# Kernel optimization log

Hardware: AMD Instinct MI355X
Metric: run time of the kernel (lower is better)

Reference implementation:

```python
import jax, jax.numpy as jnp
import numpy as np
from jax.scipy.linalg import solve_triangular

EPS = 2e-05  # module eps (only used on Cholesky failure in torch; cov is PD here since M >> N)


def setup_inputs() -> dict:
    key = jax.random.key(0)
    k1, k2, k3 = jax.random.split(key, 3)
    B, N, H, W = 8, 512, 64, 64
    return {
        "cont_feat": jax.random.normal(k1, (B, N, H, W), dtype=jnp.float32),
        "styl_feat": jax.random.normal(k2, (B, N, H, W), dtype=jnp.float32),
        "x_real": jax.random.normal(k3, (B, N, H, W), dtype=jnp.float32),
    }


def reference(cont_feat, styl_feat, x_real):
    B, N, cH, cW = cont_feat.shape
    xc = cont_feat.reshape(B, N, -1)   # [B, N, Mc]
    xs = styl_feat.reshape(B, N, -1)   # [B, N, Ms]
    # x_real is reshaped in the original but never used by whitening()

    # whitening: center, covariance, Cholesky, inv(L) @ x (as triangular solve)
    xc_c = xc - jnp.mean(xc, axis=-1, keepdims=True)
    cov_c = jnp.einsum('bnm,bkm->bnk', xc_c, xc_c) / (xc_c.shape[-1] - 1)  # [B,N,N]
    Lc = jnp.linalg.cholesky(cov_c)
    whiten = solve_triangular(Lc, xc_c, lower=True)  # == inv(Lc) @ xc_c

    # coloring: style covariance Cholesky, Ls @ whiten + style mean
    xs_mean = jnp.mean(xs, axis=-1, keepdims=True)
    xs_c = xs - xs_mean
    cov_s = jnp.einsum('bnm,bkm->bnk', xs_c, xs_c) / (xs_c.shape[-1] - 1)
    Ls = jnp.linalg.cholesky(cov_s)
    out = jnp.einsum('bnk,bkm->bnm', Ls, whiten) + xs_mean
    return out.reshape(B, N, cH, cW)
```

## Files before the change

kernel.cpp:

```cpp
#include <hip/hip_runtime.h>
#include <stdint.h>


using short8   = __attribute__((ext_vector_type(8))) short;
using short4_t = __attribute__((ext_vector_type(4))) short;
using f32x4    = __attribute__((ext_vector_type(4))) float;

#define DEVI static __device__ __forceinline__

DEVI uint16_t f32_to_bf16(float f) {
  union { float f; uint32_t u; } v{f};
  uint32_t u = v.u;
  return (uint16_t)((u + 0x7fffu + ((u >> 16) & 1u)) >> 16);
}

DEVI f32x4 mfma16(short8 a, short8 b, f32x4 c) {
  return __builtin_amdgcn_mfma_f32_16x16x32_bf16(a, b, c, 0, 0, 0);
}

typedef __attribute__((address_space(3))) uint32_t lds_u32;
typedef __attribute__((address_space(1))) const uint32_t gmem_u32;

DEVI void async_cp16(const uint16_t* g, uint16_t* l) {
  __builtin_amdgcn_global_load_lds((gmem_u32*)g, (lds_u32*)l, 16, 0, 0);
}

DEVI void stage_tile(const uint16_t* __restrict__ src, int stride,
                     uint16_t* lds, int tid) {
  int w64 = (tid >> 6) << 6;
  #pragma unroll
  for (int i = 0; i < 4; ++i) {
    int f = i * 256 + tid;
    int r = f >> 3, s = f & 7;
    int c = s ^ (r & 7);
    async_cp16(src + r * stride + c * 8, lds + (i * 256 + w64) * 8);
  }
}

DEVI short8 frag_ld(const uint16_t* lds, int r, int ch) {
  return *(const short8*)(lds + r * 64 + ((ch ^ (r & 7)) * 8));
}

__global__ __launch_bounds__(256) void k_meanconv(
    const float* __restrict__ cont, const float* __restrict__ styl,
    uint16_t* __restrict__ Yc, uint16_t* __restrict__ Ys, float* __restrict__ mus) {
  int rid = blockIdx.x;
  int row = rid & 4095;
  bool is_s = rid >= 4096;
  const float* src = (is_s ? styl : cont) + (size_t)row * 4096;
  uint16_t* dst = (is_s ? Ys : Yc) + (size_t)row * 4096;
  int tid = threadIdx.x, lane = tid & 63, w = tid >> 6;

  float4 v[4];
  #pragma unroll
  for (int i = 0; i < 4; ++i) v[i] = ((const float4*)src)[i * 256 + tid];
  float s = 0.f;
  #pragma unroll
  for (int i = 0; i < 4; ++i) s += v[i].x + v[i].y + v[i].z + v[i].w;
  #pragma unroll
  for (int off = 32; off > 0; off >>= 1) s += __shfl_down(s, off);
  __shared__ float red[4];
  if (lane == 0) red[w] = s;
  __syncthreads();
  float mean = (red[0] + red[1] + red[2] + red[3]) * (1.0f / 4096.0f);
  if (is_s && tid == 0) mus[row] = mean;

  #pragma unroll
  for (int i = 0; i < 4; ++i) {
    short4_t o;
    o[0] = (short)f32_to_bf16(v[i].x - mean);
    o[1] = (short)f32_to_bf16(v[i].y - mean);
    o[2] = (short)f32_to_bf16(v[i].z - mean);
    o[3] = (short)f32_to_bf16(v[i].w - mean);
    ((short4_t*)dst)[i * 256 + tid] = o;
  }
}

__global__ __launch_bounds__(256) void k_cov(const uint16_t* __restrict__ Y,
                                             float* __restrict__ covA) {
  int bx = blockIdx.x;
  int mat = bx / 10, q = bx % 10;
  int it = (q >= 6) ? 3 : (q >= 3) ? 2 : (q >= 1) ? 1 : 0;
  int jt = q - it * (it + 1) / 2;
  const uint16_t* A = Y + (size_t)mat * 2097152;
  float* C = covA + (size_t)mat * 262144;
  __shared__ uint16_t Al[128 * 64], Bl[128 * 64];
  int tid = threadIdx.x, lane = tid & 63, w = tid >> 6;
  int wr = w >> 1, wc = w & 1, m16 = lane & 15, q4 = lane >> 4;

  f32x4 acc[4][4] = {};
  for (int kb = 0; kb < 64; ++kb) {
    __syncthreads();
    stage_tile(A + it * 128 * 4096 + kb * 64, 4096, Al, tid);
    stage_tile(A + jt * 128 * 4096 + kb * 64, 4096, Bl, tid);
    __syncthreads();
    #pragma unroll
    for (int ks = 0; ks < 2; ++ks) {
      short8 af[4], bg[4];
      #pragma unroll
      for (int t = 0; t < 4; ++t) af[t] = frag_ld(Al, wr * 64 + t * 16 + m16, ks * 4 + q4);
      #pragma unroll
      for (int t = 0; t < 4; ++t) bg[t] = frag_ld(Bl, wc * 64 + t * 16 + m16, ks * 4 + q4);
      #pragma unroll
      for (int i2 = 0; i2 < 4; ++i2)
        #pragma unroll
        for (int j2 = 0; j2 < 4; ++j2)
          acc[i2][j2] = mfma16(af[i2], bg[j2], acc[i2][j2]);
    }
  }
  const float sc = 1.0f / 4095.0f;
  #pragma unroll
  for (int t = 0; t < 4; ++t)
    #pragma unroll
    for (int u = 0; u < 4; ++u)
      #pragma unroll
      for (int g = 0; g < 4; ++g) {
        int row = it * 128 + wr * 64 + t * 16 + q4 * 4 + g;
        int col = jt * 128 + wc * 64 + u * 16 + m16;
        C[row * 512 + col] = acc[t][u][g] * sc;
      }
}

__global__ __launch_bounds__(512) void k_chol(float* __restrict__ covA,
                                              uint16_t* __restrict__ L16) {
  int mat = blockIdx.x;
  float* C = covA + (size_t)mat * 262144;
  uint16_t* L = L16 + (size_t)mat * 262144;
  __shared__ float P[512 * 36];
  __shared__ uint16_t Pb[512 * 40];
  __shared__ uint16_t Mb[32 * 40];
  int tid = threadIdx.x, lane = tid & 63, w = tid >> 6;
  int m16 = lane & 15, q4 = lane >> 4;

  for (int j = 0; j < 16; ++j) {
    int c0 = j * 32, n = 512 - c0;

    for (int e = tid; e < n * 8; e += 512) {
      int r = e >> 3, c4 = e & 7;
      *(float4*)&P[r * 36 + c4 * 4] =
          *(const float4*)(C + (size_t)(c0 + r) * 512 + c0 + c4 * 4);
    }
    __syncthreads();

    if (w == 0) {
      if (c0 > 0) {
        f32x4 t00 = {}, t10 = {}, t11 = {};
        const uint16_t* L0 = L + (size_t)(c0 + m16) * 512;
        const uint16_t* L1r = L + (size_t)(c0 + 16 + m16) * 512;
        for (int kk = 0; kk < c0; kk += 32) {
          short8 f0 = *(const short8*)(L0 + kk + q4 * 8);
          short8 f1 = *(const short8*)(L1r + kk + q4 * 8);
          t00 = mfma16(f0, f0, t00);
          t10 = mfma16(f1, f0, t10);
          t11 = mfma16(f1, f1, t11);
        }
        #pragma unroll
        for (int g = 0; g < 4; ++g) {
          int r0 = q4 * 4 + g;
          P[r0 * 36 + m16]              -= t00[g];
          P[(16 + r0) * 36 + m16]       -= t10[g];
          P[(16 + r0) * 36 + 16 + m16]  -= t11[g];
        }
      }
      if (lane < 32) {
        int r = lane;
        float a[32];
        #pragma unroll
        for (int c4 = 0; c4 < 8; ++c4) {
          float4 v = *(const float4*)&P[r * 36 + c4 * 4];
          a[c4 * 4 + 0] = v.x; a[c4 * 4 + 1] = v.y;
          a[c4 * 4 + 2] = v.z; a[c4 * 4 + 3] = v.w;
        }
        float myinv = 0.f;
        #pragma unroll
        for (int t = 0; t < 32; ++t) {
          float pv  = __shfl(a[t], t);
          float inv = __builtin_amdgcn_rsqf(pv);
          a[t] *= inv;
          if (r == t) myinv = inv;
          float scv = a[t];
          #pragma unroll
          for (int c = t + 1; c < 32; ++c)
            a[c] -= scv * __shfl(scv, c);
        }
        float xv[32];
        #pragma unroll
        for (int c = 0; c < 32; ++c) xv[c] = (c <= r) ? a[c] : 0.0f;
        float* Cw = C + (size_t)(c0 + r) * 512 + c0;
        uint16_t* Lw = L + (size_t)(c0 + r) * 512 + c0;
        #pragma unroll
        for (int c4 = 0; c4 < 8; ++c4)
          *(float4*)(Cw + c4 * 4) = make_float4(xv[c4 * 4], xv[c4 * 4 + 1],
                                                xv[c4 * 4 + 2], xv[c4 * 4 + 3]);
        #pragma unroll
        for (int c8 = 0; c8 < 4; ++c8) {
          short8 o;
          #pragma unroll
          for (int u = 0; u < 8; ++u) o[u] = (short)f32_to_bf16(xv[c8 * 8 + u]);
          *(short8*)(Lw + c8 * 8) = o;
        }
        if (n > 32) {
          float b[32];
          #pragma unroll
          for (int c = 0; c < 32; ++c) b[c] = (c == r) ? myinv : 0.0f;
          #pragma unroll
          for (int m = 0; m < 31; ++m) {
            float coef = a[m] * myinv;
            #pragma unroll
            for (int c = 0; c <= m; ++c) {
              float v = __shfl(b[c], m);
              if (r > m) b[c] -= coef * v;
            }
          }
          uint16_t* Mw = Mb + r * 40;
          #pragma unroll
          for (int c8 = 0; c8 < 4; ++c8) {
            short8 o;
            #pragma unroll
            for (int u = 0; u < 8; ++u) o[u] = (short)f32_to_bf16(b[c8 * 8 + u]);
            *(short8*)(Mw + c8 * 8) = o;
          }
        }
      }
    } else {
      int ntiles = (n - 32) >> 4;
      const uint16_t* B0 = L + (size_t)(c0 + m16) * 512;
      const uint16_t* B1 = L + (size_t)(c0 + 16 + m16) * 512;
      for (int t = w - 1; t < ntiles; t += 7) {
        f32x4 acc0 = {}, acc1 = {};
        const uint16_t* Ar = L + (size_t)(c0 + 32 + t * 16 + m16) * 512;
        for (int kk = 0; kk < c0; kk += 32) {
          short8 af = *(const short8*)(Ar + kk + q4 * 8);
          short8 b0 = *(const short8*)(B0 + kk + q4 * 8);
          short8 b1 = *(const short8*)(B1 + kk + q4 * 8);
          acc0 = mfma16(af, b0, acc0);
          acc1 = mfma16(af, b1, acc1);
        }
        #pragma unroll
        for (int g = 0; g < 4; ++g) {
          int pr = 32 + t * 16 + q4 * 4 + g;
          float v0 = P[pr * 36 + m16]      - acc0[g];
          float v1 = P[pr * 36 + 16 + m16] - acc1[g];
          Pb[pr * 40 + m16]      = f32_to_bf16(v0);
          Pb[pr * 40 + 16 + m16] = f32_to_bf16(v1);
        }
      }
    }
    __syncthreads();

    if (n > 32) {
      int ntiles = (n - 32) >> 4;
      short8 bm0 = *(const short8*)(Mb + m16 * 40 + q4 * 8);
      short8 bm1 = *(const short8*)(Mb + (16 + m16) * 40 + q4 * 8);
      for (int t = w; t < ntiles; t += 8) {
        short8 af = *(const short8*)(Pb + (size_t)(32 + t * 16 + m16) * 40 + q4 * 8);
        f32x4 x0 = {}, x1 = {};
        x0 = mfma16(af, bm0, x0);
        x1 = mfma16(af, bm1, x1);
        #pragma unroll
        for (int g = 0; g < 4; ++g) {
          int gr = c0 + 32 + t * 16 + q4 * 4 + g;
          float v0 = x0[g], v1 = x1[g];
          C[(size_t)gr * 512 + c0 + m16]      = v0;
          C[(size_t)gr * 512 + c0 + 16 + m16] = v1;
          L[(size_t)gr * 512 + c0 + m16]      = f32_to_bf16(v0);
          L[(size_t)gr * 512 + c0 + 16 + m16] = f32_to_bf16(v1);
        }
      }
    }
  }
}

__global__ __launch_bounds__(256) void k_trinv(const float* __restrict__ covA,
                                               uint16_t* __restrict__ Ut) {
  int bx = blockIdx.x;
  int matb = bx >> 5;
  int sub = bx & 31;
  int cb = sub >> 2, colgrp = sub & 3;
  const float* Lm = covA + (size_t)matb * 262144;
  uint16_t* U = Ut + (size_t)matb * 262144;
  int tid = threadIdx.x, lane = tid & 63, w = tid >> 6;
  int j = cb * 64 + colgrp * 16 + w * 4;

  __shared__ float Bl[64 * 66];
  __shared__ float Xl[4][4][512];

  for (int rb = cb; rb < 8; ++rb) {
    float acc[4];
    #pragma unroll
    for (int c = 0; c < 4; ++c) acc[c] = ((rb * 64 + lane) == (j + c)) ? 1.0f : 0.0f;
    for (int pb = cb; pb < rb; ++pb) {
      __syncthreads();
      for (int e = tid; e < 4096; e += 256)
        Bl[(e >> 6) * 66 + (e & 63)] = Lm[(rb * 64 + (e >> 6)) * 512 + pb * 64 + (e & 63)];
      __syncthreads();
      #pragma unroll 4
      for (int m = 0; m < 64; m += 2) {
        float2 b2 = *(const float2*)&Bl[lane * 66 + m];
        #pragma unroll
        for (int c = 0; c < 4; ++c)
          acc[c] -= b2.x * Xl[w][c][pb * 64 + m] + b2.y * Xl[w][c][pb * 64 + m + 1];
      }
    }
    __syncthreads();
    for (int e = tid; e < 4096; e += 256)
      Bl[(e >> 6) * 66 + (e & 63)] = Lm[(rb * 64 + (e >> 6)) * 512 + rb * 64 + (e & 63)];
    __syncthreads();
    float invd = __builtin_amdgcn_rcpf(Bl[lane * 66 + lane]);
    #pragma unroll 1
    for (int i = 0; i < 64; ++i) {
      float bcol = Bl[lane * 66 + i];
      if (lane == i) {
        #pragma unroll
        for (int c = 0; c < 4; ++c) acc[c] *= invd;
      }
      float xi[4];
      #pragma unroll
      for (int c = 0; c < 4; ++c) xi[c] = __shfl(acc[c], i);
      if (lane > i) {
        #pragma unroll
        for (int c = 0; c < 4; ++c) acc[c] -= bcol * xi[c];
      }
    }
    #pragma unroll
    for (int c = 0; c < 4; ++c) {
      Xl[w][c][rb * 64 + lane] = acc[c];
      U[(j + c) * 512 + rb * 64 + lane] = f32_to_bf16(acc[c]);
    }
  }
}

__global__ __launch_bounds__(256) void k_tprod(const uint16_t* __restrict__ Ls16,
                                               const uint16_t* __restrict__ Ut16,
                                               uint16_t* __restrict__ T16) {
  int bx = blockIdx.x;
  int b = bx / 10, q = bx % 10;
  int it = (q >= 6) ? 3 : (q >= 3) ? 2 : (q >= 1) ? 1 : 0;
  int jt = q - it * (it + 1) / 2;
  const uint16_t* A = Ls16 + (size_t)b * 262144;
  const uint16_t* B = Ut16 + (size_t)b * 262144;
  uint16_t* C = T16 + (size_t)b * 262144;
  __shared__ uint16_t Al[128 * 64], Bl[128 * 64];
  int tid = threadIdx.x, lane = tid & 63, w = tid >> 6;
  int wr = w >> 1, wc = w & 1, m16 = lane & 15, q4 = lane >> 4;

  f32x4 acc[4][4] = {};
  for (int kb = jt * 2; kb < (it + 1) * 2; ++kb) {
    __syncthreads();
    stage_tile(A + it * 128 * 512 + kb * 64, 512, Al, tid);
    stage_tile(B + jt * 128 * 512 + kb * 64, 512, Bl, tid);
    __syncthreads();
    #pragma unroll
    for (int ks = 0; ks < 2; ++ks) {
      short8 af[4], bg[4];
      #pragma unroll
      for (int t = 0; t < 4; ++t) af[t] = frag_ld(Al, wr * 64 + t * 16 + m16, ks * 4 + q4);
      #pragma unroll
      for (int t = 0; t < 4; ++t) bg[t] = frag_ld(Bl, wc * 64 + t * 16 + m16, ks * 4 + q4);
      #pragma unroll
      for (int i2 = 0; i2 < 4; ++i2)
        #pragma unroll
        for (int j2 = 0; j2 < 4; ++j2)
          acc[i2][j2] = mfma16(af[i2], bg[j2], acc[i2][j2]);
    }
  }
  #pragma unroll
  for (int t = 0; t < 4; ++t)
    #pragma unroll
    for (int u = 0; u < 4; ++u)
      #pragma unroll
      for (int g = 0; g < 4; ++g) {
        int row = it * 128 + wr * 64 + t * 16 + q4 * 4 + g;
        int col = jt * 128 + wc * 64 + u * 16 + m16;
        C[row * 512 + col] = f32_to_bf16(acc[t][u][g]);
      }
}

__global__ __launch_bounds__(256) void k_out(const uint16_t* __restrict__ T16,
                                             const uint16_t* __restrict__ Ycb,
                                             const float* __restrict__ mus,
                                             float* __restrict__ out) {
  int bx = blockIdx.x;
  int b = bx >> 7, q = bx & 127;
  int it = q >> 5, mt = q & 31;
  int m0 = mt * 128;
  const uint16_t* Tm = T16 + (size_t)b * 262144;
  const uint16_t* Y = Ycb + (size_t)b * 2097152;
  __shared__ uint16_t Al[128 * 64];
  __shared__ uint16_t Bt[128 * 68];
  int tid = threadIdx.x, lane = tid & 63, w = tid >> 6;
  int wr = w >> 1, wc = w & 1, m16 = lane & 15, q4 = lane >> 4;

  f32x4 acc[4][4] = {};
  int kbmax = (it + 1) * 2;
  for (int kb = 0; kb < kbmax; ++kb) {
    __syncthreads();
    stage_tile(Tm + it * 128 * 512 + kb * 64, 512, Al, tid);
    #pragma unroll
    for (int rep = 0; rep < 2; ++rep) {
      int task = rep * 256 + tid;
      int n8 = task & 15, kp = task >> 4;
      const uint16_t* p = Y + (size_t)(kb * 64 + 2 * kp) * 4096 + m0 + n8 * 8;
      short8 a0 = *(const short8*)p;
      short8 a1 = *(const short8*)(p + 4096);
      #pragma unroll
      for (int u = 0; u < 8; ++u) {
        int n = n8 * 8 + u;
        uint32_t pk = (uint32_t)(uint16_t)a0[u] | ((uint32_t)(uint16_t)a1[u] << 16);
        *(uint32_t*)(Bt + n * 68 + 2 * kp) = pk;
      }
    }
    __syncthreads();
    #pragma unroll
    for (int ks = 0; ks < 2; ++ks) {
      short8 af[4], bg[4];
      #pragma unroll
      for (int t = 0; t < 4; ++t) af[t] = frag_ld(Al, wr * 64 + t * 16 + m16, ks * 4 + q4);
      #pragma unroll
      for (int t = 0; t < 4; ++t) {
        int n = wc * 64 + t * 16 + m16;
        int ko = ks * 4 + q4;
        short8 bb;
        ((short4_t*)&bb)[0] = *(const short4_t*)(Bt + n * 68 + ko * 8);
        ((short4_t*)&bb)[1] = *(const short4_t*)(Bt + n * 68 + ko * 8 + 4);
        bg[t] = bb;
      }
      #pragma unroll
      for (int i2 = 0; i2 < 4; ++i2)
        #pragma unroll
        for (int j2 = 0; j2 < 4; ++j2)
          acc[i2][j2] = mfma16(af[i2], bg[j2], acc[i2][j2]);
    }
  }
  #pragma unroll
  for (int t = 0; t < 4; ++t)
    #pragma unroll
    for (int g = 0; g < 4; ++g) {
      int row = it * 128 + wr * 64 + t * 16 + q4 * 4 + g;
      float mu = mus[b * 512 + row];
      #pragma unroll
      for (int u = 0; u < 4; ++u) {
        int col = m0 + wc * 64 + u * 16 + m16;
        out[(size_t)(b * 512 + row) * 4096 + col] = acc[t][u][g] + mu;
      }
    }
}

extern "C" void kernel_launch(void* const* d_in, const int* in_sizes, int n_in,
                              void* d_out, int out_size, void* d_ws, size_t ws_size,
                              hipStream_t stream) {
  const float* cont = (const float*)d_in[0];
  const float* styl = (const float*)d_in[1];
  float* out = (float*)d_out;
  char* ws = (char*)d_ws;

  uint16_t* Ycb  = (uint16_t*)(ws);
  float*    covA = (float*)(ws + 67108864);
  uint16_t* L16  = (uint16_t*)(ws + 83886080);
  uint16_t* Ut16 = (uint16_t*)(ws + 92274688);
  uint16_t* T16  = (uint16_t*)(ws + 96468992);
  float*    mus  = (float*)(ws + 100663296);

  uint16_t* Ysb  = Ycb + 16777216;
  uint16_t* Ls16 = L16 + 8 * 262144;

  hipMemsetAsync((void*)L16, 0, 16777216, stream);

  k_meanconv<<<dim3(8192), dim3(256), 0, stream>>>(cont, styl, Ycb, Ysb, mus);
  k_cov     <<<dim3(160),  dim3(256), 0, stream>>>(Ycb, covA);
  k_chol    <<<dim3(16),   dim3(512), 0, stream>>>(covA, L16);
  k_trinv   <<<dim3(256),  dim3(256), 0, stream>>>(covA, Ut16);
  k_tprod   <<<dim3(80),   dim3(256), 0, stream>>>(Ls16, Ut16, T16);
  k_out     <<<dim3(1024), dim3(256), 0, stream>>>(T16, Ycb, mus, out);
}
```

Measured before the change: 726.8 us.

## Restructure Cholesky panel: drop full panel staging, batch tiles per wave, prefetch

```diff
diff --git a/kernel.cpp b/kernel.cpp
--- a/kernel.cpp
+++ b/kernel.cpp
@@ -126,48 +126,68 @@
   int mat = blockIdx.x;
   float* C = covA + (size_t)mat * 262144;
   uint16_t* L = L16 + (size_t)mat * 262144;
-  __shared__ float P[512 * 36];
+  __shared__ float Pd[32 * 36];
   __shared__ uint16_t Pb[512 * 40];
   __shared__ uint16_t Mb[32 * 40];
   int tid = threadIdx.x, lane = tid & 63, w = tid >> 6;
   int m16 = lane & 15, q4 = lane >> 4;
 
   for (int j = 0; j < 16; ++j) {
-    int c0 = j * 32, n = 512 - c0;
-
-    for (int e = tid; e < n * 8; e += 512) {
-      int r = e >> 3, c4 = e & 7;
-      *(float4*)&P[r * 36 + c4 * 4] =
-          *(const float4*)(C + (size_t)(c0 + r) * 512 + c0 + c4 * 4);
-    }
-    __syncthreads();
+    int c0 = j * 32;
+    int nb = (480 - 32 * j) >> 4;
+
+    int trow[5]; int myn = 0;
+    #pragma unroll
+    for (int i = 0; i < 5; ++i) {
+      int t = (w - 1) + i * 7;
+      trow[i] = c0 + 32 + t * 16;
+      if (w >= 1 && t < nb) myn = i + 1;
+    }
 
     if (w == 0) {
+      float4 pdv[4];
+      #pragma unroll
+      for (int i2 = 0; i2 < 4; ++i2) {
+        int e = i2 * 64 + lane, r = e >> 3, c4 = e & 7;
+        pdv[i2] = *(const float4*)(C + (size_t)(c0 + r) * 512 + c0 + c4 * 4);
+      }
+      f32x4 t00 = {}, t10 = {}, t11 = {};
       if (c0 > 0) {
-        f32x4 t00 = {}, t10 = {}, t11 = {};
-        const uint16_t* L0 = L + (size_t)(c0 + m16) * 512;
-        const uint16_t* L1r = L + (size_t)(c0 + 16 + m16) * 512;
+        const uint16_t* L0  = L + (size_t)(c0 + m16) * 512 + q4 * 8;
+        const uint16_t* L1r = L + (size_t)(c0 + 16 + m16) * 512 + q4 * 8;
+        short8 f0 = *(const short8*)(L0);
+        short8 f1 = *(const short8*)(L1r);
+        short8 g0, g1;
         for (int kk = 0; kk < c0; kk += 32) {
-          short8 f0 = *(const short8*)(L0 + kk + q4 * 8);
-          short8 f1 = *(const short8*)(L1r + kk + q4 * 8);
+          bool more = (kk + 32) < c0;
+          if (more) {
+            g0 = *(const short8*)(L0 + kk + 32);
+            g1 = *(const short8*)(L1r + kk + 32);
+          }
           t00 = mfma16(f0, f0, t00);
           t10 = mfma16(f1, f0, t10);
           t11 = mfma16(f1, f1, t11);
-        }
-        #pragma unroll
-        for (int g = 0; g < 4; ++g) {
-          int r0 = q4 * 4 + g;
-          P[r0 * 36 + m16]              -= t00[g];
-          P[(16 + r0) * 36 + m16]       -= t10[g];
-          P[(16 + r0) * 36 + 16 + m16]  -= t11[g];
-        }
+          if (more) { f0 = g0; f1 = g1; }
+        }
+      }
+      #pragma unroll
+      for (int i2 = 0; i2 < 4; ++i2) {
+        int e = i2 * 64 + lane, r = e >> 3, c4 = e & 7;
+        *(float4*)&Pd[r * 36 + c4 * 4] = pdv[i2];
+      }
+      #pragma unroll
+      for (int g = 0; g < 4; ++g) {
+        int r0 = q4 * 4 + g;
+        Pd[r0 * 36 + m16]             -= t00[g];
+        Pd[(16 + r0) * 36 + m16]      -= t10[g];
+        Pd[(16 + r0) * 36 + 16 + m16] -= t11[g];
       }
       if (lane < 32) {
         int r = lane;
         float a[32];
         #pragma unroll
         for (int c4 = 0; c4 < 8; ++c4) {
-          float4 v = *(const float4*)&P[r * 36 + c4 * 4];
+          float4 v = *(const float4*)&Pd[r * 36 + c4 * 4];
           a[c4 * 4 + 0] = v.x; a[c4 * 4 + 1] = v.y;
           a[c4 * 4 + 2] = v.z; a[c4 * 4 + 3] = v.w;
         }
@@ -199,7 +219,7 @@
           for (int u = 0; u < 8; ++u) o[u] = (short)f32_to_bf16(xv[c8 * 8 + u]);
           *(short8*)(Lw + c8 * 8) = o;
         }
-        if (n > 32) {
+        if (nb > 0) {
           float b[32];
           #pragma unroll
           for (int c = 0; c < 32; ++c) b[c] = (c == r) ? myinv : 0.0f;
@@ -222,44 +242,73 @@
           }
         }
       }
-    } else {
-      int ntiles = (n - 32) >> 4;
-      const uint16_t* B0 = L + (size_t)(c0 + m16) * 512;
-      const uint16_t* B1 = L + (size_t)(c0 + 16 + m16) * 512;
-      for (int t = w - 1; t < ntiles; t += 7) {
-        f32x4 acc0 = {}, acc1 = {};
-        const uint16_t* Ar = L + (size_t)(c0 + 32 + t * 16 + m16) * 512;
+    } else if (myn > 0) {
+      float po0[5][4], po1[5][4];
+      #pragma unroll
+      for (int i = 0; i < 5; ++i) if (i < myn) {
+        #pragma unroll
+        for (int g = 0; g < 4; ++g) {
+          const float* cr = C + (size_t)(trow[i] + q4 * 4 + g) * 512 + c0;
+          po0[i][g] = cr[m16];
+          po1[i][g] = cr[16 + m16];
+        }
+      }
+      f32x4 acc0[5] = {}, acc1[5] = {};
+      if (c0 > 0) {
+        const uint16_t* Lb0 = L + (size_t)(c0 + m16) * 512 + q4 * 8;
+        const uint16_t* Lb1 = L + (size_t)(c0 + 16 + m16) * 512 + q4 * 8;
+        short8 cb0 = *(const short8*)(Lb0);
+        short8 cb1 = *(const short8*)(Lb1);
+        short8 ca[5], na[5];
+        short8 nb0c, nb1c;
+        #pragma unroll
+        for (int i = 0; i < 5; ++i) if (i < myn)
+          ca[i] = *(const short8*)(L + (size_t)(trow[i] + m16) * 512 + q4 * 8);
         for (int kk = 0; kk < c0; kk += 32) {
-          short8 af = *(const short8*)(Ar + kk + q4 * 8);
-          short8 b0 = *(const short8*)(B0 + kk + q4 * 8);
-          short8 b1 = *(const short8*)(B1 + kk + q4 * 8);
-          acc0 = mfma16(af, b0, acc0);
-          acc1 = mfma16(af, b1, acc1);
-        }
+          bool more = (kk + 32) < c0;
+          if (more) {
+            nb0c = *(const short8*)(Lb0 + kk + 32);
+            nb1c = *(const short8*)(Lb1 + kk + 32);
+            #pragma unroll
+            for (int i = 0; i < 5; ++i) if (i < myn)
+              na[i] = *(const short8*)(L + (size_t)(trow[i] + m16) * 512 + kk + 32 + q4 * 8);
+          }
+          #pragma unroll
+          for (int i = 0; i < 5; ++i) if (i < myn) {
+            acc0[i] = mfma16(ca[i], cb0, acc0[i]);
+            acc1[i] = mfma16(ca[i], cb1, acc1[i]);
+          }
+          if (more) {
+            cb0 = nb0c; cb1 = nb1c;
+            #pragma unroll
+            for (int i = 0; i < 5; ++i) ca[i] = na[i];
+          }
+        }
+      }
+      #pragma unroll
+      for (int i = 0; i < 5; ++i) if (i < myn) {
         #pragma unroll
         for (int g = 0; g < 4; ++g) {
-          int pr = 32 + t * 16 + q4 * 4 + g;
-          float v0 = P[pr * 36 + m16]      - acc0[g];
-          float v1 = P[pr * 36 + 16 + m16] - acc1[g];
-          Pb[pr * 40 + m16]      = f32_to_bf16(v0);
-          Pb[pr * 40 + 16 + m16] = f32_to_bf16(v1);
-        }
-      }
-    }
-    __syncthreads();
-
-    if (n > 32) {
-      int ntiles = (n - 32) >> 4;
+          int pr = trow[i] - c0 + q4 * 4 + g;
+          Pb[pr * 40 + m16]      = f32_to_bf16(po0[i][g] - acc0[i][g]);
+          Pb[pr * 40 + 16 + m16] = f32_to_bf16(po1[i][g] - acc1[i][g]);
+        }
+      }
+    }
+    __syncthreads();
+
+    if (myn > 0) {
       short8 bm0 = *(const short8*)(Mb + m16 * 40 + q4 * 8);
       short8 bm1 = *(const short8*)(Mb + (16 + m16) * 40 + q4 * 8);
-      for (int t = w; t < ntiles; t += 8) {
-        short8 af = *(const short8*)(Pb + (size_t)(32 + t * 16 + m16) * 40 + q4 * 8);
+      #pragma unroll
+      for (int i = 0; i < 5; ++i) if (i < myn) {
+        short8 af = *(const short8*)(Pb + (size_t)(trow[i] - c0 + m16) * 40 + q4 * 8);
         f32x4 x0 = {}, x1 = {};
         x0 = mfma16(af, bm0, x0);
         x1 = mfma16(af, bm1, x1);
         #pragma unroll
         for (int g = 0; g < 4; ++g) {
-          int gr = c0 + 32 + t * 16 + q4 * 4 + g;
+          int gr = trow[i] + q4 * 4 + g;
           float v0 = x0[g], v1 = x1[g];
           C[(size_t)gr * 512 + c0 + m16]      = v0;
           C[(size_t)gr * 512 + c0 + 16 + m16] = v1;
@@ -268,6 +317,7 @@
         }
       }
     }
+    __syncthreads();
   }
 }
 
```

After: 794.7 us. 1.09x slower.

## Split-K covariance GEMM, fuse block inverse into Cholesky panel, prefetch L loads

Applied to the files above, without the earlier changes.

```diff
diff --git a/kernel.cpp b/kernel.cpp
--- a/kernel.cpp
+++ b/kernel.cpp
@@ -76,10 +76,12 @@
   }
 }
 
-__global__ __launch_bounds__(256) void k_cov(const uint16_t* __restrict__ Y,
-                                             float* __restrict__ covA) {
+__global__ __launch_bounds__(256) void k_covp(const uint16_t* __restrict__ Y,
+                                              float* __restrict__ covA,
+                                              float* __restrict__ covB) {
   int bx = blockIdx.x;
-  int mat = bx / 10, q = bx % 10;
+  int split = bx & 1, rest = bx >> 1;
+  int mat = rest / 10, q = rest % 10;
   int it = (q >= 6) ? 3 : (q >= 3) ? 2 : (q >= 1) ? 1 : 0;
   int jt = q - it * (it + 1) / 2;
   const uint16_t* A = Y + (size_t)mat * 2097152;
@@ -89,7 +91,7 @@
   int wr = w >> 1, wc = w & 1, m16 = lane & 15, q4 = lane >> 4;
 
   f32x4 acc[4][4] = {};
-  for (int kb = 0; kb < 64; ++kb) {
+  for (int kb = split * 32; kb < split * 32 + 32; ++kb) {
     __syncthreads();
     stage_tile(A + it * 128 * 4096 + kb * 64, 4096, Al, tid);
     stage_tile(A + jt * 128 * 4096 + kb * 64, 4096, Bl, tid);
@@ -109,16 +111,44 @@
     }
   }
   const float sc = 1.0f / 4095.0f;
-  #pragma unroll
-  for (int t = 0; t < 4; ++t)
-    #pragma unroll
-    for (int u = 0; u < 4; ++u)
-      #pragma unroll
-      for (int g = 0; g < 4; ++g) {
-        int row = it * 128 + wr * 64 + t * 16 + q4 * 4 + g;
-        int col = jt * 128 + wc * 64 + u * 16 + m16;
-        C[row * 512 + col] = acc[t][u][g] * sc;
-      }
+  if (split == 0) {
+    #pragma unroll
+    for (int t = 0; t < 4; ++t)
+      #pragma unroll
+      for (int u = 0; u < 4; ++u)
+        #pragma unroll
+        for (int g = 0; g < 4; ++g) {
+          int row = it * 128 + wr * 64 + t * 16 + q4 * 4 + g;
+          int col = jt * 128 + wc * 64 + u * 16 + m16;
+          C[row * 512 + col] = acc[t][u][g] * sc;
+        }
+  } else {
+    float* Bp = covB + (size_t)rest * 16384;
+    #pragma unroll
+    for (int t = 0; t < 4; ++t)
+      #pragma unroll
+      for (int u = 0; u < 4; ++u)
+        #pragma unroll
+        for (int g = 0; g < 4; ++g) {
+          int row = wr * 64 + t * 16 + q4 * 4 + g;
+          int col = wc * 64 + u * 16 + m16;
+          Bp[row * 128 + col] = acc[t][u][g] * sc;
+        }
+  }
+}
+
+__global__ __launch_bounds__(256) void k_covfix(float* __restrict__ covA,
+                                                const float* __restrict__ covB) {
+  int bx = blockIdx.x;
+  int mat = bx / 10, q = bx % 10;
+  int it = (q >= 6) ? 3 : (q >= 3) ? 2 : (q >= 1) ? 1 : 0;
+  int jt = q - it * (it + 1) / 2;
+  float* C = covA + (size_t)mat * 262144;
+  const float* Bp = covB + (size_t)bx * 16384;
+  for (int e = threadIdx.x; e < 16384; e += 256) {
+    int r = e >> 7, c = e & 127;
+    C[(it * 128 + r) * 512 + jt * 128 + c] += Bp[e];
+  }
 }
 
 __global__ __launch_bounds__(512) void k_chol(float* __restrict__ covA,
@@ -145,14 +175,18 @@
     if (w == 0) {
       if (c0 > 0) {
         f32x4 t00 = {}, t10 = {}, t11 = {};
-        const uint16_t* L0 = L + (size_t)(c0 + m16) * 512;
-        const uint16_t* L1r = L + (size_t)(c0 + 16 + m16) * 512;
+        const uint16_t* L0  = L + (size_t)(c0 + m16) * 512 + q4 * 8;
+        const uint16_t* L1r = L + (size_t)(c0 + 16 + m16) * 512 + q4 * 8;
+        short8 f0 = *(const short8*)(L0);
+        short8 f1 = *(const short8*)(L1r);
         for (int kk = 0; kk < c0; kk += 32) {
-          short8 f0 = *(const short8*)(L0 + kk + q4 * 8);
-          short8 f1 = *(const short8*)(L1r + kk + q4 * 8);
+          int kn = (kk + 32 < c0) ? kk + 32 : kk;
+          short8 g0 = *(const short8*)(L0 + kn);
+          short8 g1 = *(const short8*)(L1r + kn);
           t00 = mfma16(f0, f0, t00);
           t10 = mfma16(f1, f0, t10);
           t11 = mfma16(f1, f1, t11);
+          f0 = g0; f1 = g1;
         }
         #pragma unroll
         for (int g = 0; g < 4; ++g) {
@@ -164,6 +198,7 @@
       }
       if (lane < 32) {
         int r = lane;
+        bool needM = (n > 32);
         float a[32];
         #pragma unroll
         for (int c4 = 0; c4 < 8; ++c4) {
@@ -171,17 +206,27 @@
           a[c4 * 4 + 0] = v.x; a[c4 * 4 + 1] = v.y;
           a[c4 * 4 + 2] = v.z; a[c4 * 4 + 3] = v.w;
         }
-        float myinv = 0.f;
+        float s_[32], Mrow[32];
+        #pragma unroll
+        for (int c = 0; c < 32; ++c) { s_[c] = 0.f; Mrow[c] = 0.f; }
         #pragma unroll
         for (int t = 0; t < 32; ++t) {
           float pv  = __shfl(a[t], t);
           float inv = __builtin_amdgcn_rsqf(pv);
           a[t] *= inv;
-          if (r == t) myinv = inv;
           float scv = a[t];
           #pragma unroll
           for (int c = t + 1; c < 32; ++c)
             a[c] -= scv * __shfl(scv, c);
+          if (needM) {
+            #pragma unroll
+            for (int c = 0; c <= t; ++c) {
+              float fin = (((c == t) ? 1.0f : 0.0f) - s_[c]) * inv;
+              float mvt = __shfl(fin, t);
+              if (r == t) Mrow[c] = fin;
+              if (r > t) s_[c] += a[t] * mvt;
+            }
+          }
         }
         float xv[32];
         #pragma unroll
@@ -199,42 +244,37 @@
           for (int u = 0; u < 8; ++u) o[u] = (short)f32_to_bf16(xv[c8 * 8 + u]);
           *(short8*)(Lw + c8 * 8) = o;
         }
-        if (n > 32) {
-          float b[32];
-          #pragma unroll
-          for (int c = 0; c < 32; ++c) b[c] = (c == r) ? myinv : 0.0f;
-          #pragma unroll
-          for (int m = 0; m < 31; ++m) {
-            float coef = a[m] * myinv;
-            #pragma unroll
-            for (int c = 0; c <= m; ++c) {
-              float v = __shfl(b[c], m);
-              if (r > m) b[c] -= coef * v;
-            }
-          }
+        if (needM) {
           uint16_t* Mw = Mb + r * 40;
           #pragma unroll
           for (int c8 = 0; c8 < 4; ++c8) {
             short8 o;
             #pragma unroll
-            for (int u = 0; u < 8; ++u) o[u] = (short)f32_to_bf16(b[c8 * 8 + u]);
+            for (int u = 0; u < 8; ++u) o[u] = (short)f32_to_bf16(Mrow[c8 * 8 + u]);
             *(short8*)(Mw + c8 * 8) = o;
           }
         }
       }
     } else {
       int ntiles = (n - 32) >> 4;
-      const uint16_t* B0 = L + (size_t)(c0 + m16) * 512;
-      const uint16_t* B1 = L + (size_t)(c0 + 16 + m16) * 512;
+      const uint16_t* B0 = L + (size_t)(c0 + m16) * 512 + q4 * 8;
+      const uint16_t* B1 = L + (size_t)(c0 + 16 + m16) * 512 + q4 * 8;
       for (int t = w - 1; t < ntiles; t += 7) {
         f32x4 acc0 = {}, acc1 = {};
-        const uint16_t* Ar = L + (size_t)(c0 + 32 + t * 16 + m16) * 512;
-        for (int kk = 0; kk < c0; kk += 32) {
-          short8 af = *(const short8*)(Ar + kk + q4 * 8);
-          short8 b0 = *(const short8*)(B0 + kk + q4 * 8);
-          short8 b1 = *(const short8*)(B1 + kk + q4 * 8);
-          acc0 = mfma16(af, b0, acc0);
-          acc1 = mfma16(af, b1, acc1);
+        const uint16_t* Ar = L + (size_t)(c0 + 32 + t * 16 + m16) * 512 + q4 * 8;
+        if (c0 > 0) {
+          short8 af = *(const short8*)(Ar);
+          short8 b0 = *(const short8*)(B0);
+          short8 b1 = *(const short8*)(B1);
+          for (int kk = 0; kk < c0; kk += 32) {
+            int kn = (kk + 32 < c0) ? kk + 32 : kk;
+            short8 nf = *(const short8*)(Ar + kn);
+            short8 n0 = *(const short8*)(B0 + kn);
+            short8 n1 = *(const short8*)(B1 + kn);
+            acc0 = mfma16(af, b0, acc0);
+            acc1 = mfma16(af, b1, acc1);
+            af = nf; b0 = n0; b1 = n1;
+          }
         }
         #pragma unroll
         for (int g = 0; g < 4; ++g) {
@@ -460,14 +500,15 @@
   uint16_t* Ut16 = (uint16_t*)(ws + 92274688);
   uint16_t* T16  = (uint16_t*)(ws + 96468992);
   float*    mus  = (float*)(ws + 100663296);
+  float*    covB = (float*)(ws + 83886080);
 
   uint16_t* Ysb  = Ycb + 16777216;
   uint16_t* Ls16 = L16 + 8 * 262144;
 
+  k_meanconv<<<dim3(8192), dim3(256), 0, stream>>>(cont, styl, Ycb, Ysb, mus);
+  k_covp    <<<dim3(320),  dim3(256), 0, stream>>>(Ycb, covA, covB);
+  k_covfix  <<<dim3(160),  dim3(256), 0, stream>>>(covA, covB);
   hipMemsetAsync((void*)L16, 0, 16777216, stream);
-
-  k_meanconv<<<dim3(8192), dim3(256), 0, stream>>>(cont, styl, Ycb, Ysb, mus);
-  k_cov     <<<dim3(160),  dim3(256), 0, stream>>>(Ycb, covA);
   k_chol    <<<dim3(16),   dim3(512), 0, stream>>>(covA, L16);
   k_trinv   <<<dim3(256),  dim3(256), 0, stream>>>(covA, Ut16);
   k_tprod   <<<dim3(80),   dim3(256), 0, stream>>>(Ls16, Ut16, T16);
```

Result: slower. 927.3 us (+27.6%).
